# Optimization experiments

Measured on AMD Instinct MI355X. Metric: run time of the kernel, lower is better.

The kernel has to match this reference:

```python
import jax, jax.numpy as jnp
import numpy as np

NI = 256        # in_channels
QK = NI // 8    # query/key channels = 32
BS, H, W = 4, 64, 64


def setup_inputs() -> dict:
    key = jax.random.key(0)
    ks = jax.random.split(key, 8)
    x = jax.random.normal(ks[0], (BS, NI, H, W), dtype=jnp.float32)
    # 1x1 conv weights stored as [out_ch, in_ch] (kernel is 1x1)
    wq = jax.random.normal(ks[1], (QK, NI), dtype=jnp.float32) * (1.0 / np.sqrt(NI))
    bq = jnp.zeros((QK,), dtype=jnp.float32)
    wk = jax.random.normal(ks[2], (QK, NI), dtype=jnp.float32) * (1.0 / np.sqrt(NI))
    bk = jnp.zeros((QK,), dtype=jnp.float32)
    wv = jax.random.normal(ks[3], (NI, NI), dtype=jnp.float32) * (1.0 / np.sqrt(NI))
    bv = jnp.zeros((NI,), dtype=jnp.float32)
    # gamma is zero-init in the module; use small random values so the
    # attention branch actually contributes (post-training state).
    gamma = jax.random.normal(ks[4], (1, NI, 1, 1), dtype=jnp.float32) * 0.1
    return {"x": x, "wq": wq, "bq": bq, "wk": wk, "bk": bk,
            "wv": wv, "bv": bv, "gamma": gamma}


def reference(x, wq, bq, wk, bk, wv, bv, gamma):
    bs, c, h, w = x.shape
    n = h * w
    xf = x.reshape(bs, c, n)                       # [bs, c, N]
    # 1x1 convs == per-pixel linear maps over channels
    q = jnp.einsum('oc,bcn->bno', wq, xf) + bq     # [bs, N, qk]
    k = jnp.einsum('oc,bcn->bon', wk, xf) + bk[None, :, None]  # [bs, qk, N]
    v = jnp.einsum('oc,bcn->bon', wv, xf) + bv[None, :, None]  # [bs, c, N]
    attn = jax.nn.softmax(jnp.einsum('bnq,bqm->bnm', q, k), axis=-1)  # [bs, N, N]
    out = jnp.einsum('bcm,bnm->bcn', v, attn)      # value @ attn^T
    out = out.reshape(bs, c, h, w)
    return gamma * out + x
```

## Files before the change

### kernel.cpp

```cpp
#include <hip/hip_runtime.h>
#include <cstdint>
#include <cstddef>

#define NI   256
#define QKC  32
#define BS   4
#define NPIX 4096
#define LOG2E 1.4426950408889634f

typedef __bf16 bf16x8 __attribute__((ext_vector_type(8)));
typedef __bf16 bf16x4 __attribute__((ext_vector_type(4)));
typedef float  f32x16 __attribute__((ext_vector_type(16)));

__device__ inline f32x16 zero16() {
    f32x16 z;
    #pragma unroll
    for (int i = 0; i < 16; ++i) z[i] = 0.f;
    return z;
}

__global__ __launch_bounds__(256) void wconv_pack(
    const float* __restrict__ wq, const float* __restrict__ wk,
    const float* __restrict__ wv, __bf16* __restrict__ wpk)
{
    int f = blockIdx.x * 256 + threadIdx.x;
    int otl = f >> 10, rem = f & 1023;
    int kk = rem >> 6, h = (rem >> 5) & 1, l31 = rem & 31;
    int och = otl * 32 + l31, c0 = kk * 16 + 8 * h;
    const float* src = och < 32 ? wq + och * NI + c0
                     : och < 64 ? wk + (och - 32) * NI + c0
                                : wv + (och - 64) * NI + c0;
    float4 x0 = *(const float4*)src;
    float4 x1 = *(const float4*)(src + 4);
    __align__(16) __bf16 o8[8] = {
        (__bf16)x0.x, (__bf16)x0.y, (__bf16)x0.z, (__bf16)x0.w,
        (__bf16)x1.x, (__bf16)x1.y, (__bf16)x1.z, (__bf16)x1.w};
    *(uint4*)(wpk + (size_t)f * 8) = *(const uint4*)o8;
}

__global__ __launch_bounds__(256) void qkv_mfma(
    const float* __restrict__ x, const __bf16* __restrict__ wpk,
    const float* __restrict__ bq, const float* __restrict__ bk,
    const float* __restrict__ bv,
    __bf16* __restrict__ qpk, __bf16* __restrict__ kpk, __bf16* __restrict__ vpk)
{
    __shared__ __align__(16) __bf16 xT[32][264];
    __shared__ float bls[320];

    const int t = threadIdx.x, w = t >> 6, lane = t & 63;
    const int l31 = lane & 31, h = lane >> 5;
    const int b = blockIdx.y, n0 = blockIdx.x * 32, kt = blockIdx.x;

    for (int i = t; i < 320; i += 256)
        bls[i] = i < 32 ? bq[i] : i < 64 ? bk[i - 32] : bv[i - 64];

    {
        int n4 = (t & 7) * 4, cb = (t >> 3) * 8;
        float4 xv[8];
        #pragma unroll
        for (int j = 0; j < 8; ++j)
            xv[j] = *(const float4*)(x + ((size_t)(b * NI) + cb + j) * NPIX + n0 + n4);
        #pragma unroll
        for (int i = 0; i < 4; ++i) {
            __align__(16) __bf16 r8[8];
            #pragma unroll
            for (int j = 0; j < 8; ++j) r8[j] = (__bf16)((&xv[j].x)[i]);
            *(uint4*)&xT[n4 + i][cb] = *(const uint4*)r8;
        }
    }
    __syncthreads();

    f32x16 acc[3] = {zero16(), zero16(), zero16()};
    #pragma unroll 4
    for (int kk = 0; kk < 16; ++kk) {
        bf16x8 xf = *(const bf16x8*)&xT[l31][kk * 16 + 8 * h];
        #pragma unroll
        for (int jj = 0; jj < 3; ++jj) {
            int otl = w + 4 * jj;
            if (otl < 10) {
                bf16x8 wf = *(const bf16x8*)(wpk + (size_t)((otl * 16 + kk) * 64 + 32 * h + l31) * 8);
                acc[jj] = __builtin_amdgcn_mfma_f32_32x32x16_bf16(wf, xf, acc[jj], 0, 0, 0);
            }
        }
    }
    __syncthreads();

    __bf16 (*vT)[264] = xT;
    #pragma unroll
    for (int jj = 0; jj < 3; ++jj) {
        int otl = w + 4 * jj;
        if (otl >= 2 && otl < 10) {
            #pragma unroll
            for (int qd = 0; qd < 4; ++qd) {
                int c0v = (otl - 2) * 32 + 8 * qd + 4 * h;
                __align__(8) __bf16 q4[4];
                #pragma unroll
                for (int i = 0; i < 4; ++i)
                    q4[i] = (__bf16)(acc[jj][4 * qd + i] + bls[64 + c0v + i]);
                *(uint2*)&vT[l31][c0v] = *(const uint2*)q4;
            }
        }
    }
    #pragma unroll
    for (int jj = 0; jj < 3; ++jj) {
        int otl = w + 4 * jj;
        if (otl == 0) {
            #pragma unroll
            for (int kc = 0; kc < 2; ++kc) {
                __align__(16) __bf16 hi8[8], lo8[8];
                #pragma unroll
                for (int j = 0; j < 8; ++j) {
                    int r = 8 * kc + j;
                    int och = (r & 3) + 8 * (r >> 2) + 4 * h;
                    float val = (acc[jj][r] + bls[och]) * LOG2E;
                    __bf16 hh = (__bf16)val;
                    hi8[j] = hh;
                    lo8[j] = (__bf16)(val - (float)hh);
                }
                size_t base = ((((size_t)(b * 128 + kt) * 2 + 0) * 2 + kc) * 2 + h) * 32 + l31;
                *(uint4*)(qpk + base * 8) = *(const uint4*)hi8;
                size_t basel = ((((size_t)(b * 128 + kt) * 2 + 1) * 2 + kc) * 2 + h) * 32 + l31;
                *(uint4*)(qpk + basel * 8) = *(const uint4*)lo8;
            }
        } else if (otl == 1) {
            #pragma unroll
            for (int kc = 0; kc < 2; ++kc) {
                __align__(16) __bf16 k8[8];
                #pragma unroll
                for (int j = 0; j < 8; ++j) {
                    int r = 8 * kc + j;
                    int och = (r & 3) + 8 * (r >> 2) + 4 * h;
                    k8[j] = (__bf16)(acc[jj][r] + bls[32 + och]);
                }
                size_t base = (((size_t)(b * 128 + kt) * 2 + kc) * 2 + h) * 32 + l31;
                *(uint4*)(kpk + base * 8) = *(const uint4*)k8;
            }
        }
    }
    __syncthreads();

    #pragma unroll
    for (int kc = 0; kc < 2; ++kc)
        #pragma unroll
        for (int hh = 0; hh < 2; ++hh) {
            __align__(16) __bf16 f8[8];
            #pragma unroll
            for (int j = 0; j < 8; ++j) f8[j] = vT[16 * kc + 8 * hh + j][t];
            size_t base = (((size_t)(b * 128 + kt) * 2 + kc) * 2 + hh) * 256 + t;
            *(uint4*)(vpk + base * 8) = *(const uint4*)f8;
        }
}

__global__ __launch_bounds__(512, 4) void attn_mfma(
    const __bf16* __restrict__ qpk, const __bf16* __restrict__ kpk,
    const __bf16* __restrict__ vpk,
    __bf16* __restrict__ Opart, float* __restrict__ dpart)
{
    __shared__ __align__(16) __bf16 pt_f[4][2][4][64][8];
    __shared__ float dwave[8][32];

    const int t = threadIdx.x;
    const int b = blockIdx.x & 3, ksp = blockIdx.x >> 2;
    const int n0 = blockIdx.y * 64;
    const int w = t >> 6, lane = t & 63, l31 = lane & 31, h = lane >> 5;
    const int q = w & 3, sr = q & 1, sc = q >> 1, pp = w >> 2;
    const int kt0 = ksp * 64;

    const int qt = 2 * blockIdx.y + sr;
    bf16x8 qf[2][2];
    #pragma unroll
    for (int hl = 0; hl < 2; ++hl)
        #pragma unroll
        for (int kc = 0; kc < 2; ++kc)
            qf[hl][kc] = *(const bf16x8*)(qpk +
                (((((size_t)(b * 128 + qt) * 2 + hl) * 2 + kc) * 2 + h) * 32 + l31) * 8);

    auto kload = [&](int ktile, int kc) {
        return *(const bf16x8*)(kpk +
            ((((size_t)(b * 128 + ktile) * 2 + kc) * 2 + h) * 32 + l31) * 8);
    };
    auto vload = [&](int ktile, int kc) {
        return *(const bf16x8*)(vpk +
            ((((size_t)(b * 128 + ktile) * 2 + kc) * 2 + h) * 256 + 32 * w + l31) * 8);
    };

    f32x16 a0 = zero16(), a1 = zero16();
    float dacc = 0.f;

    auto smma = [&](bf16x8 kh0, bf16x8 kh1) {
        f32x16 s = zero16();
        __builtin_amdgcn_s_setprio(1);
        s = __builtin_amdgcn_mfma_f32_32x32x16_bf16(kh0, qf[0][0], s, 0, 0, 0);
        s = __builtin_amdgcn_mfma_f32_32x32x16_bf16(kh1, qf[0][1], s, 0, 0, 0);
        s = __builtin_amdgcn_mfma_f32_32x32x16_bf16(kh0, qf[1][0], s, 0, 0, 0);
        s = __builtin_amdgcn_mfma_f32_32x32x16_bf16(kh1, qf[1][1], s, 0, 0, 0);
        __builtin_amdgcn_s_setprio(0);
        return s;
    };

    auto sfin = [&](const f32x16& s, int buf) {
        unsigned xw[8], xs[8];
        #pragma unroll
        for (int i = 0; i < 8; ++i) {
            float e0 = __builtin_amdgcn_exp2f(s[2 * i]);
            float e1 = __builtin_amdgcn_exp2f(s[2 * i + 1]);
            dacc += e0 + e1;
            __align__(4) __bf16 pr[2] = {(__bf16)e0, (__bf16)e1};
            xw[i] = *(const unsigned*)pr;
        }
        #pragma unroll
        for (int i = 0; i < 8; ++i) xs[i] = __shfl_xor(xw[i], 32);
        const bool hi = (h != 0);
        __align__(16) unsigned f0[4], f1[4];
        f0[0] = hi ? xs[2] : xw[0];  f0[1] = hi ? xs[3] : xw[1];
        f0[2] = hi ? xw[2] : xs[0];  f0[3] = hi ? xw[3] : xs[1];
        f1[0] = hi ? xs[6] : xw[4];  f1[1] = hi ? xs[7] : xw[5];
        f1[2] = hi ? xw[6] : xs[4];  f1[3] = hi ? xw[7] : xs[5];
        *(uint4*)&pt_f[buf][sr][2 * sc + 0][lane][0] = *(const uint4*)f0;
        *(uint4*)&pt_f[buf][sr][2 * sc + 1][lane][0] = *(const uint4*)f1;
    };

    auto pvblock = [&](int mt, const bf16x8 (*vf)[2]) {
        const int buf = mt & 3;
        __builtin_amdgcn_s_setprio(1);
        #pragma unroll
        for (int i = 0; i < 2; ++i)
            #pragma unroll
            for (int kc = 0; kc < 2; ++kc) {
                const int s2 = 2 * i + kc;
                bf16x8 pa0 = *(const bf16x8*)&pt_f[buf][0][s2][lane][0];
                bf16x8 pa1 = *(const bf16x8*)&pt_f[buf][1][s2][lane][0];
                a0 = __builtin_amdgcn_mfma_f32_32x32x16_bf16(pa0, vf[i][kc], a0, 0, 0, 0);
                a1 = __builtin_amdgcn_mfma_f32_32x32x16_bf16(pa1, vf[i][kc], a1, 0, 0, 0);
            }
        __builtin_amdgcn_s_setprio(0);
    };

    bf16x8 kh0 = kload(kt0 + 2 * pp + sc, 0), kh1 = kload(kt0 + 2 * pp + sc, 1);
    {
        f32x16 s = smma(kh0, kh1);
        sfin(s, pp);
    }
    kh0 = kload(kt0 + 2 * (2 + pp) + sc, 0);
    kh1 = kload(kt0 + 2 * (2 + pp) + sc, 1);
    __syncthreads();

    for (int j = 0; j < 16; ++j) {
        f32x16 s;
        if (j < 15) s = smma(kh0, kh1);

        bf16x8 vfa[2][2];
        #pragma unroll
        for (int i = 0; i < 2; ++i)
            #pragma unroll
            for (int kc = 0; kc < 2; ++kc)
                vfa[i][kc] = vload(kt0 + 4 * j + i, kc);

        if (j < 14) {
            const int mtsn = 2 * j + 4 + pp;
            kh0 = kload(kt0 + 2 * mtsn + sc, 0);
            kh1 = kload(kt0 + 2 * mtsn + sc, 1);
        }
        if (j < 15) sfin(s, (2 * j + 2 + pp) & 3);

        bf16x8 vfb[2][2];
        #pragma unroll
        for (int i = 0; i < 2; ++i)
            #pragma unroll
            for (int kc = 0; kc < 2; ++kc)
                vfb[i][kc] = vload(kt0 + 4 * j + 2 + i, kc);

        pvblock(2 * j, vfa);
        pvblock(2 * j + 1, vfb);
        __syncthreads();
    }

    float dtot = dacc + __shfl_xor(dacc, 32);
    if (lane < 32) dwave[w][l31] = dtot;
    __syncthreads();
    if (w < 2 && lane < 32) {
        float dsum = dwave[w][l31] + dwave[w + 2][l31]
                   + dwave[w + 4][l31] + dwave[w + 6][l31];
        dpart[((size_t)(ksp * BS + b)) * NPIX + n0 + 32 * w + l31] = dsum;
    }

    size_t obase = (((size_t)(ksp * BS + b)) * NI + 32 * w + l31) * NPIX + n0;
    #pragma unroll
    for (int rq = 0; rq < 4; ++rq) {
        int nn = 8 * rq + 4 * h;
        __align__(8) __bf16 t0[4], t1[4];
        #pragma unroll
        for (int i = 0; i < 4; ++i) {
            t0[i] = (__bf16)a0[4 * rq + i];
            t1[i] = (__bf16)a1[4 * rq + i];
        }
        *(uint2*)(Opart + obase + nn)      = *(const uint2*)t0;
        *(uint2*)(Opart + obase + 32 + nn) = *(const uint2*)t1;
    }
}

__global__ __launch_bounds__(256) void combine(
    const float* __restrict__ x, const float* __restrict__ gamma,
    const __bf16* __restrict__ Opart, const float* __restrict__ dpart,
    float* __restrict__ out)
{
    int idx = (blockIdx.x * 256 + threadIdx.x) * 4;
    int n = idx & (NPIX - 1);
    int c = (idx >> 12) & (NI - 1);
    int b = idx >> 20;

    size_t o0 = (((size_t)(0 * BS + b)) * NI + c) * NPIX + n;
    size_t o1 = (((size_t)(1 * BS + b)) * NI + c) * NPIX + n;
    bf16x4 p0 = *(const bf16x4*)(Opart + o0);
    bf16x4 p1 = *(const bf16x4*)(Opart + o1);
    float4 da = *(const float4*)(dpart + ((size_t)(0 * BS + b)) * NPIX + n);
    float4 db = *(const float4*)(dpart + ((size_t)(1 * BS + b)) * NPIX + n);
    size_t xb = ((size_t)(b * NI) + c) * NPIX + n;
    float4 xv = *(const float4*)(x + xb);
    float g = gamma[c];

    float4 r;
    r.x = g * (((float)p0[0] + (float)p1[0]) / (da.x + db.x)) + xv.x;
    r.y = g * (((float)p0[1] + (float)p1[1]) / (da.y + db.y)) + xv.y;
    r.z = g * (((float)p0[2] + (float)p1[2]) / (da.z + db.z)) + xv.z;
    r.w = g * (((float)p0[3] + (float)p1[3]) / (da.w + db.w)) + xv.w;
    *(float4*)(out + xb) = r;
}

extern "C" void kernel_launch(void* const* d_in, const int* in_sizes, int n_in,
                              void* d_out, int out_size, void* d_ws, size_t ws_size,
                              hipStream_t stream)
{
    const float* x     = (const float*)d_in[0];
    const float* wq    = (const float*)d_in[1];
    const float* bq    = (const float*)d_in[2];
    const float* wk    = (const float*)d_in[3];
    const float* bk    = (const float*)d_in[4];
    const float* wv    = (const float*)d_in[5];
    const float* bv    = (const float*)d_in[6];
    const float* gamma = (const float*)d_in[7];
    float* out = (float*)d_out;

    const size_t WPK = (size_t)10240 * 8;
    const size_t QPK = (size_t)BS * 128 * 2 * 2 * 2 * 32 * 8;
    const size_t KPK = (size_t)BS * 128 * 2 * 2 * 32 * 8;
    const size_t VPK = (size_t)BS * 128 * 2 * 2 * 256 * 8;
    const size_t OSZ = (size_t)2 * BS * NI * NPIX;
    __bf16* wpk   = (__bf16*)d_ws;
    __bf16* qpk   = wpk + WPK;
    __bf16* kpk   = qpk + QPK;
    __bf16* vpk   = kpk + KPK;
    __bf16* Opart = vpk + VPK;
    float*  dpart = (float*)(Opart + OSZ);

    wconv_pack<<<dim3(40), 256, 0, stream>>>(wq, wk, wv, wpk);
    qkv_mfma<<<dim3(NPIX / 32, BS), 256, 0, stream>>>(x, wpk, bq, bk, bv, qpk, kpk, vpk);
    attn_mfma<<<dim3(8, 64), 512, 0, stream>>>(qpk, kpk, vpk, Opart, dpart);
    combine<<<dim3(BS * NI * NPIX / 1024), 256, 0, stream>>>(x, gamma, Opart, dpart, out);
}
```

Baseline: 159.2 us.

## Split attention blocks over value channels with 4-wave blocks, each computing all score tiles

The attention kernel moves from 512-thread blocks, where two wave groups split the score tiles, to 256-thread blocks that each cover half of the value channels and launch twice as many blocks. Each wave now computes both score tiles per iteration itself and interleaves the two softmax/exp stages with the score MFMAs. The goal is more, smaller blocks for better occupancy and scheduling. The cost is that every score/exp computation is duplicated across the two channel halves, and K is loaded twice as often.

```diff
diff --git a/kernel.cpp b/kernel.cpp
--- a/kernel.cpp
+++ b/kernel.cpp
@@ -151,19 +151,19 @@
         }
 }
 
-__global__ __launch_bounds__(512, 4) void attn_mfma(
+__global__ __launch_bounds__(256, 4) void attn_mfma(
     const __bf16* __restrict__ qpk, const __bf16* __restrict__ kpk,
     const __bf16* __restrict__ vpk,
     __bf16* __restrict__ Opart, float* __restrict__ dpart)
 {
     __shared__ __align__(16) __bf16 pt_f[4][2][4][64][8];
-    __shared__ float dwave[8][32];
+    __shared__ float dwave[4][32];
 
     const int t = threadIdx.x;
-    const int b = blockIdx.x & 3, ksp = blockIdx.x >> 2;
+    const int b = blockIdx.x & 3, cs = (blockIdx.x >> 2) & 1, ksp = blockIdx.x >> 3;
     const int n0 = blockIdx.y * 64;
     const int w = t >> 6, lane = t & 63, l31 = lane & 31, h = lane >> 5;
-    const int q = w & 3, sr = q & 1, sc = q >> 1, pp = w >> 2;
+    const int sr = w & 1, sc = w >> 1;
     const int kt0 = ksp * 64;
 
     const int qt = 2 * blockIdx.y + sr;
@@ -181,7 +181,8 @@
     };
     auto vload = [&](int ktile, int kc) {
         return *(const bf16x8*)(vpk +
-            ((((size_t)(b * 128 + ktile) * 2 + kc) * 2 + h) * 256 + 32 * w + l31) * 8);
+            ((((size_t)(b * 128 + ktile) * 2 + kc) * 2 + h) * 256
+             + 128 * cs + 32 * w + l31) * 8);
     };
 
     f32x16 a0 = zero16(), a1 = zero16();
@@ -199,25 +200,41 @@
     };
 
     auto sfin = [&](const f32x16& s, int buf) {
-        unsigned xw[8], xs[8];
-        #pragma unroll
-        for (int i = 0; i < 8; ++i) {
-            float e0 = __builtin_amdgcn_exp2f(s[2 * i]);
-            float e1 = __builtin_amdgcn_exp2f(s[2 * i + 1]);
-            dacc += e0 + e1;
-            __align__(4) __bf16 pr[2] = {(__bf16)e0, (__bf16)e1};
-            xw[i] = *(const unsigned*)pr;
-        }
-        #pragma unroll
-        for (int i = 0; i < 8; ++i) xs[i] = __shfl_xor(xw[i], 32);
         const bool hi = (h != 0);
-        __align__(16) unsigned f0[4], f1[4];
-        f0[0] = hi ? xs[2] : xw[0];  f0[1] = hi ? xs[3] : xw[1];
-        f0[2] = hi ? xw[2] : xs[0];  f0[3] = hi ? xw[3] : xs[1];
-        f1[0] = hi ? xs[6] : xw[4];  f1[1] = hi ? xs[7] : xw[5];
-        f1[2] = hi ? xw[6] : xs[4];  f1[3] = hi ? xw[7] : xs[5];
-        *(uint4*)&pt_f[buf][sr][2 * sc + 0][lane][0] = *(const uint4*)f0;
-        *(uint4*)&pt_f[buf][sr][2 * sc + 1][lane][0] = *(const uint4*)f1;
+        {
+            unsigned xw[4], xs[4];
+            #pragma unroll
+            for (int i = 0; i < 4; ++i) {
+                float e0 = __builtin_amdgcn_exp2f(s[2 * i]);
+                float e1 = __builtin_amdgcn_exp2f(s[2 * i + 1]);
+                dacc += e0 + e1;
+                __align__(4) __bf16 pr[2] = {(__bf16)e0, (__bf16)e1};
+                xw[i] = *(const unsigned*)pr;
+            }
+            #pragma unroll
+            for (int i = 0; i < 4; ++i) xs[i] = __shfl_xor(xw[i], 32);
+            __align__(16) unsigned f0[4];
+            f0[0] = hi ? xs[2] : xw[0];  f0[1] = hi ? xs[3] : xw[1];
+            f0[2] = hi ? xw[2] : xs[0];  f0[3] = hi ? xw[3] : xs[1];
+            *(uint4*)&pt_f[buf][sr][2 * sc + 0][lane][0] = *(const uint4*)f0;
+        }
+        {
+            unsigned xw[4], xs[4];
+            #pragma unroll
+            for (int i = 0; i < 4; ++i) {
+                float e0 = __builtin_amdgcn_exp2f(s[2 * i + 8]);
+                float e1 = __builtin_amdgcn_exp2f(s[2 * i + 9]);
+                dacc += e0 + e1;
+                __align__(4) __bf16 pr[2] = {(__bf16)e0, (__bf16)e1};
+                xw[i] = *(const unsigned*)pr;
+            }
+            #pragma unroll
+            for (int i = 0; i < 4; ++i) xs[i] = __shfl_xor(xw[i], 32);
+            __align__(16) unsigned f1[4];
+            f1[0] = hi ? xs[2] : xw[0];  f1[1] = hi ? xs[3] : xw[1];
+            f1[2] = hi ? xw[2] : xs[0];  f1[3] = hi ? xw[3] : xs[1];
+            *(uint4*)&pt_f[buf][sr][2 * sc + 1][lane][0] = *(const uint4*)f1;
+        }
     };
 
     auto pvblock = [&](int mt, const bf16x8 (*vf)[2]) {
@@ -236,18 +253,17 @@
         __builtin_amdgcn_s_setprio(0);
     };
 
-    bf16x8 kh0 = kload(kt0 + 2 * pp + sc, 0), kh1 = kload(kt0 + 2 * pp + sc, 1);
-    {
-        f32x16 s = smma(kh0, kh1);
-        sfin(s, pp);
-    }
-    kh0 = kload(kt0 + 2 * (2 + pp) + sc, 0);
-    kh1 = kload(kt0 + 2 * (2 + pp) + sc, 1);
+    bf16x8 ka0 = kload(kt0 + sc, 0),     ka1 = kload(kt0 + sc, 1);
+    bf16x8 kb0 = kload(kt0 + 2 + sc, 0), kb1 = kload(kt0 + 2 + sc, 1);
+    { f32x16 s = smma(ka0, ka1); sfin(s, 0); }
+    { f32x16 s = smma(kb0, kb1); sfin(s, 1); }
+    ka0 = kload(kt0 + 4 + sc, 0); ka1 = kload(kt0 + 4 + sc, 1);
+    kb0 = kload(kt0 + 6 + sc, 0); kb1 = kload(kt0 + 6 + sc, 1);
     __syncthreads();
 
     for (int j = 0; j < 16; ++j) {
-        f32x16 s;
-        if (j < 15) s = smma(kh0, kh1);
+        f32x16 sa, sb;
+        if (j < 15) sa = smma(ka0, ka1);
 
         bf16x8 vfa[2][2];
         #pragma unroll
@@ -256,12 +272,17 @@
             for (int kc = 0; kc < 2; ++kc)
                 vfa[i][kc] = vload(kt0 + 4 * j + i, kc);
 
+        if (j < 15) {
+            sfin(sa, (2 * j + 2) & 3);
+            sb = smma(kb0, kb1);
+        }
         if (j < 14) {
-            const int mtsn = 2 * j + 4 + pp;
-            kh0 = kload(kt0 + 2 * mtsn + sc, 0);
-            kh1 = kload(kt0 + 2 * mtsn + sc, 1);
-        }
-        if (j < 15) sfin(s, (2 * j + 2 + pp) & 3);
+            ka0 = kload(kt0 + 4 * j + 8 + sc, 0);
+            ka1 = kload(kt0 + 4 * j + 8 + sc, 1);
+            kb0 = kload(kt0 + 4 * j + 10 + sc, 0);
+            kb1 = kload(kt0 + 4 * j + 10 + sc, 1);
+        }
+        if (j < 15) sfin(sb, (2 * j + 3) & 3);
 
         bf16x8 vfb[2][2];
         #pragma unroll
@@ -278,13 +299,12 @@
     float dtot = dacc + __shfl_xor(dacc, 32);
     if (lane < 32) dwave[w][l31] = dtot;
     __syncthreads();
-    if (w < 2 && lane < 32) {
-        float dsum = dwave[w][l31] + dwave[w + 2][l31]
-                   + dwave[w + 4][l31] + dwave[w + 6][l31];
+    if (cs == 0 && w < 2 && lane < 32) {
+        float dsum = dwave[w][l31] + dwave[w + 2][l31];
         dpart[((size_t)(ksp * BS + b)) * NPIX + n0 + 32 * w + l31] = dsum;
     }
 
-    size_t obase = (((size_t)(ksp * BS + b)) * NI + 32 * w + l31) * NPIX + n0;
+    size_t obase = (((size_t)(ksp * BS + b)) * NI + 128 * cs + 32 * w + l31) * NPIX + n0;
     #pragma unroll
     for (int rq = 0; rq < 4; ++rq) {
         int nn = 8 * rq + 4 * h;
@@ -355,6 +375,6 @@
 
     wconv_pack<<<dim3(40), 256, 0, stream>>>(wq, wk, wv, wpk);
     qkv_mfma<<<dim3(NPIX / 32, BS), 256, 0, stream>>>(x, wpk, bq, bk, bv, qpk, kpk, vpk);
-    attn_mfma<<<dim3(8, 64), 512, 0, stream>>>(qpk, kpk, vpk, Opart, dpart);
+    attn_mfma<<<dim3(16, 64), 256, 0, stream>>>(qpk, kpk, vpk, Opart, dpart);
     combine<<<dim3(BS * NI * NPIX / 1024), 256, 0, stream>>>(x, gamma, Opart, dpart, out);
 }
```

New measurement: 168.6 us. +5.9%, slower.
